# Kernel tuning notes

Hardware: AMD Instinct MI355X
Metric: run time of the kernel (lower is better)

The kernel has to match this reference:

```python
import jax, jax.numpy as jnp
import numpy as np

B, T, DIM, H = 2, 2048, 512, 8
EPS = 1e-6


def setup_inputs() -> dict:
    key = jax.random.key(0)
    ks = jax.random.split(key, 6)
    scale = 0.05  # keep activations in a sane range for softmax/elu
    return {
        "x": jax.random.normal(ks[0], (B, T, DIM), dtype=jnp.float32),
        "Wq": jax.random.normal(ks[1], (DIM, DIM), dtype=jnp.float32) * scale,
        "Wk": jax.random.normal(ks[2], (DIM, DIM), dtype=jnp.float32) * scale,
        "Wv": jax.random.normal(ks[3], (DIM, DIM), dtype=jnp.float32) * scale,
        "Wo": jax.random.normal(ks[4], (DIM, DIM), dtype=jnp.float32) * scale,
        "bo": jax.random.normal(ks[5], (DIM,), dtype=jnp.float32) * scale,
    }


def reference(x, Wq, Wk, Wv, Wo, bo):
    b, t, dim = x.shape
    h = H
    d = dim // h
    # projections (nn.Linear: x @ W.T)
    q = x @ Wq.T
    k = x @ Wk.T
    v = x @ Wv.T
    mh = lambda z: z.reshape(b, t, h, d).transpose(0, 2, 1, 3)  # [b,h,t,d]
    q, k, v = mh(q), mh(k), mh(v)
    # causal linear attention with buckets = n (bucket size 1, no shift)
    q = jax.nn.softmax(q, axis=-1)
    k = jax.nn.elu(k) + 1.0  # psi
    k_cumsum = jnp.cumsum(k, axis=2)                       # [b,h,t,d]
    context = jnp.einsum('bhnd,bhne->bhnde', k, v)         # per-position outer products
    context = jnp.cumsum(context, axis=2)                  # causal prefix sum, [b,h,t,d,d]
    context = context / (k_cumsum[..., None] + EPS)        # safe_div
    attn = jnp.einsum('bhnd,bhnde->bhne', q, context)      # [b,h,t,d]
    out = attn.transpose(0, 2, 1, 3).reshape(b, t, dim)
    return out @ Wo.T + bo
```

## Files before the change

### kernel.cpp

```cpp
#include <hip/hip_runtime.h>

#define T_SEQ 2048
#define DIMM 512
#define NH 8
#define HD 64
#define BB 2
#define CHUNK 64
#define NCHUNK 32
#define EPSV 1e-6f
#define LDST 72
#define CST 132

typedef __attribute__((ext_vector_type(8))) short bf16x8;
typedef __attribute__((ext_vector_type(4))) short s16x4;
typedef __attribute__((ext_vector_type(4))) float f32x4;

static __device__ inline short f2bf(float f) {
    union { float f; unsigned u; } v; v.f = f;
    unsigned r = v.u + 0x7FFFu + ((v.u >> 16) & 1u);
    return (short)(r >> 16);
}
static __device__ inline float bf2f(short s) {
    union { unsigned u; float f; } v; v.u = ((unsigned)(unsigned short)s) << 16;
    return v.f;
}
static __device__ __forceinline__ void gload_lds16(const void* g, void* l) {
    __builtin_amdgcn_global_load_lds(
        (__attribute__((address_space(1))) void*)g,
        (__attribute__((address_space(3))) void*)l, 16, 0, 0);
}

__global__ __launch_bounds__(256) void convert_kernel(
    const float* __restrict__ x, const float* __restrict__ Wq,
    const float* __restrict__ Wk, const float* __restrict__ Wv,
    const float* __restrict__ Wo,
    short* __restrict__ xb, short* __restrict__ Wcat, short* __restrict__ Wob)
{
    const int u = blockIdx.x * 256 + threadIdx.x;
    const float* src; short* dst;
    if (u < 262144) {
        src = x + (size_t)u * 8; dst = xb + (size_t)u * 8;
    } else {
        const int v = u - 262144;
        const int o = (v & 32767) * 8;
        if (v < 32768)       { src = Wq + o; dst = Wcat + o; }
        else if (v < 65536)  { src = Wk + o; dst = Wcat + 262144 + o; }
        else if (v < 98304)  { src = Wv + o; dst = Wcat + 524288 + o; }
        else                 { src = Wo + o; dst = Wob + o; }
    }
    const float4 a = *(const float4*)src;
    const float4 b = *(const float4*)(src + 4);
    *(bf16x8*)dst = (bf16x8){f2bf(a.x), f2bf(a.y), f2bf(a.z), f2bf(a.w),
                             f2bf(b.x), f2bf(b.y), f2bf(b.z), f2bf(b.w)};
}

__global__ __launch_bounds__(256) void proj_mfma_kernel(
    const short* __restrict__ xb, const short* __restrict__ Wcat,
    short* __restrict__ Qs, short* __restrict__ Kbf,
    short* __restrict__ Ktb, short* __restrict__ Vt)
{
    __shared__ short S[64 * 64 + 128 * 64];
    short* As = S;
    short* Bs = S + 4096;
    short* Cs = S;
    const int m0 = blockIdx.x * 64;
    const int n0 = blockIdx.y * 128;
    const int which = blockIdx.y >> 2;
    const int tid = threadIdx.x;
    const int lane = tid & 63, w = tid >> 6;
    const int wr = w >> 1, wc = w & 1;
    const int fr = lane & 15, fg = lane >> 4;
    const int lr = lane >> 3, lc = (lane & 7) * 8;
    f32x4 acc[2][4] = {};
    for (int k0 = 0; k0 < DIMM; k0 += 64) {
        #pragma unroll
        for (int it = 0; it < 2; it++) {
            const int r0 = w * 16 + it * 8;
            gload_lds16(xb + (size_t)(m0 + r0 + lr) * DIMM + k0 + lc, &As[r0 * 64]);
        }
        #pragma unroll
        for (int it = 0; it < 4; it++) {
            const int r0 = w * 32 + it * 8;
            gload_lds16(Wcat + (size_t)(n0 + r0 + lr) * DIMM + k0 + lc, &Bs[r0 * 64]);
        }
        __syncthreads();
        #pragma unroll
        for (int ks = 0; ks < 2; ks++) {
            bf16x8 af[2], bfr[4];
            #pragma unroll
            for (int i = 0; i < 2; i++)
                af[i] = *(const bf16x8*)&As[(wr * 32 + i * 16 + fr) * 64 + ks * 32 + fg * 8];
            #pragma unroll
            for (int j = 0; j < 4; j++)
                bfr[j] = *(const bf16x8*)&Bs[(wc * 64 + j * 16 + fr) * 64 + ks * 32 + fg * 8];
            #pragma unroll
            for (int i = 0; i < 2; i++)
                #pragma unroll
                for (int j = 0; j < 4; j++)
                    acc[i][j] = __builtin_amdgcn_mfma_f32_16x16x32_bf16(af[i], bfr[j], acc[i][j], 0, 0, 0);
        }
        __syncthreads();
    }
    #pragma unroll
    for (int i = 0; i < 2; i++)
        #pragma unroll
        for (int j = 0; j < 4; j++)
            #pragma unroll
            for (int reg = 0; reg < 4; reg++) {
                float val = acc[i][j][reg];
                if (which == 1) val = (val > 0.f) ? (val + 1.f) : __expf(val);
                Cs[(wr * 32 + i * 16 + fg * 4 + reg) * CST + wc * 64 + j * 16 + fr] = f2bf(val);
            }
    __syncthreads();

    const int b = m0 >> 11, t0 = m0 & (T_SEQ - 1);
    if (which == 0) {
        if (tid < 128) {
            const int r = tid & 63, hh = tid >> 6;
            const int head = (blockIdx.y & 3) * 2 + hh;
            s16x4 seg[16];
            #pragma unroll
            for (int s = 0; s < 16; s++) seg[s] = *(const s16x4*)&Cs[r * CST + hh * 64 + s * 4];
            float mx = -1e30f;
            #pragma unroll
            for (int s = 0; s < 16; s++)
                #pragma unroll
                for (int k = 0; k < 4; k++) mx = fmaxf(mx, bf2f(seg[s][k]));
            float sum = 0.f;
            #pragma unroll
            for (int s = 0; s < 16; s++)
                #pragma unroll
                for (int k = 0; k < 4; k++) sum += __expf(bf2f(seg[s][k]) - mx);
            const float inv = 1.f / sum;
            short* qp = Qs + (((size_t)(b * NH + head)) * T_SEQ + t0 + r) * HD;
            #pragma unroll
            for (int s = 0; s < 16; s += 2) {
                bf16x8 o;
                #pragma unroll
                for (int k = 0; k < 4; k++) o[k] = f2bf(__expf(bf2f(seg[s][k]) - mx) * inv);
                #pragma unroll
                for (int k = 0; k < 4; k++) o[4 + k] = f2bf(__expf(bf2f(seg[s + 1][k]) - mx) * inv);
                *(bf16x8*)(qp + s * 4) = o;
            }
        }
    } else if (which == 1) {
        if (tid < 128) {
            const int r = tid & 63, hh = tid >> 6;
            const int head = (blockIdx.y & 3) * 2 + hh;
            short* kp = Kbf + (((size_t)(b * NH + head)) * T_SEQ + t0 + r) * HD;
            #pragma unroll
            for (int s = 0; s < 8; s++) {
                const s16x4 a = *(const s16x4*)&Cs[r * CST + hh * 64 + s * 8];
                const s16x4 bq = *(const s16x4*)&Cs[r * CST + hh * 64 + s * 8 + 4];
                *(bf16x8*)(kp + s * 8) = (bf16x8){a[0], a[1], a[2], a[3], bq[0], bq[1], bq[2], bq[3]};
            }
        }
        {
            const int c = tid & 127, half = tid >> 7;
            const int head = (blockIdx.y & 3) * 2 + (c >> 6);
            const int d = c & 63;
            short* ktp = Ktb + (((size_t)(b * NH + head)) * HD + d) * T_SEQ + t0 + half * 32;
            #pragma unroll
            for (int s = 0; s < 4; s++) {
                bf16x8 o;
                #pragma unroll
                for (int k = 0; k < 8; k++) o[k] = Cs[(half * 32 + s * 8 + k) * CST + c];
                *(bf16x8*)(ktp + s * 8) = o;
            }
        }
    } else {
        const int c = tid & 127, half = tid >> 7;
        const int head = (blockIdx.y & 3) * 2 + (c >> 6);
        const int e = c & 63;
        short* vtp = Vt + (((size_t)(b * NH + head)) * HD + e) * T_SEQ + t0 + half * 32;
        #pragma unroll
        for (int s = 0; s < 4; s++) {
            bf16x8 o;
            #pragma unroll
            for (int k = 0; k < 8; k++) o[k] = Cs[(half * 32 + s * 8 + k) * CST + c];
            *(bf16x8*)(vtp + s * 8) = o;
        }
    }
}

__global__ __launch_bounds__(256) void chunk_sum_kernel(
    const short* __restrict__ Ktb, const short* __restrict__ Vt,
    float* __restrict__ Schunk, float* __restrict__ kchunk)
{
    __shared__ short VtL[64 * LDST];
    __shared__ short KtL[64 * LDST];
    __shared__ float ksp[4][64];
    const int bh = blockIdx.x >> 5, c = blockIdx.x & 31;
    const int tid = threadIdx.x;
    const int lane = tid & 63, w = tid >> 6;
    const int fr = lane & 15, fg = lane >> 4;
    #pragma unroll
    for (int it = 0; it < 2; it++) {
        const int qi = it * 256 + tid;
        const int r = qi >> 3, c8 = (qi & 7) * 8;
        *(bf16x8*)&VtL[r * LDST + c8] =
            *(const bf16x8*)(Vt + ((size_t)(bh * HD) + r) * T_SEQ + c * CHUNK + c8);
        *(bf16x8*)&KtL[r * LDST + c8] =
            *(const bf16x8*)(Ktb + ((size_t)(bh * HD) + r) * T_SEQ + c * CHUNK + c8);
    }
    __syncthreads();
    f32x4 acc[4] = {};
    #pragma unroll
    for (int ks = 0; ks < 2; ks++) {
        const bf16x8 av = *(const bf16x8*)&VtL[(w * 16 + fr) * LDST + ks * 32 + fg * 8];
        #pragma unroll
        for (int j = 0; j < 4; j++) {
            const bf16x8 bk = *(const bf16x8*)&KtL[(j * 16 + fr) * LDST + ks * 32 + fg * 8];
            acc[j] = __builtin_amdgcn_mfma_f32_16x16x32_bf16(av, bk, acc[j], 0, 0, 0);
        }
    }
    float* Sout = Schunk + ((size_t)bh * NCHUNK + c) * 4096;
    #pragma unroll
    for (int j = 0; j < 4; j++)
        #pragma unroll
        for (int reg = 0; reg < 4; reg++)
            Sout[(w * 16 + fg * 4 + reg) * 64 + j * 16 + fr] = acc[j][reg];
    float ps = 0.f;
    #pragma unroll
    for (int t = 0; t < 16; t++) ps += bf2f(KtL[lane * LDST + w * 16 + t]);
    ksp[w][lane] = ps;
    __syncthreads();
    if (tid < 64)
        kchunk[((size_t)bh * NCHUNK + c) * 64 + tid] =
            ksp[0][tid] + ksp[1][tid] + ksp[2][tid] + ksp[3][tid];
}

__global__ __launch_bounds__(256) void scan_kernel(float* __restrict__ Schunk,
                                                   float* __restrict__ kchunk)
{
    const int gid = blockIdx.x * 256 + threadIdx.x;
    if (blockIdx.x < 256) {
        const int bh = gid >> 12, i = gid & 4095;
        float run = 0.f;
        float* p = Schunk + (size_t)bh * NCHUNK * 4096 + i;
        for (int c = 0; c < NCHUNK; c++) { const float tv = p[c * 4096]; p[c * 4096] = run; run += tv; }
    } else {
        const int idx = gid - 65536;
        const int bh = idx >> 6, d = idx & 63;
        float run = 0.f;
        float* p = kchunk + (size_t)bh * NCHUNK * 64 + d;
        for (int c = 0; c < NCHUNK; c++) { const float tv = p[c * 64]; p[c * 64] = run; run += tv; }
    }
}

__global__ __launch_bounds__(256) void intra_kernel(
    const short* __restrict__ Qs, const short* __restrict__ Kbf,
    const short* __restrict__ Vt, const float* __restrict__ Schunk,
    const float* __restrict__ kchunk, short* __restrict__ attnb)
{
    __shared__ short B1[64 * LDST];
    __shared__ short B2[64 * LDST];
    __shared__ short KL[64 * LDST];
    __shared__ short VtL[64 * LDST];
    __shared__ short QnL[64 * LDST];
    __shared__ float gsum[4][64];
    __shared__ float kpre[64];
    const int bh = blockIdx.x >> 5, c = blockIdx.x & 31;
    const int tid = threadIdx.x;
    const int lane = tid & 63, w = tid >> 6;
    const int fr = lane & 15, fg = lane >> 4;
    const size_t tdbase = ((size_t)bh * T_SEQ + c * CHUNK) * HD;
    #pragma unroll
    for (int it = 0; it < 2; it++) {
        const int qi = it * 256 + tid;
        const int r = qi >> 3, c8 = (qi & 7) * 8;
        *(bf16x8*)&B1[r * LDST + c8]  = *(const bf16x8*)(Qs + tdbase + r * HD + c8);
        *(bf16x8*)&KL[r * LDST + c8]  = *(const bf16x8*)(Kbf + tdbase + r * HD + c8);
        *(bf16x8*)&VtL[r * LDST + c8] =
            *(const bf16x8*)(Vt + ((size_t)(bh * HD) + r) * T_SEQ + c * CHUNK + c8);
    }
    {
        const float* Sp = Schunk + ((size_t)bh * NCHUNK + c) * 4096;
        #pragma unroll
        for (int it = 0; it < 4; it++) {
            const int qi = it * 256 + tid;
            const int r = qi >> 4, c4 = (qi & 15) * 4;
            const float4 v = *(const float4*)(Sp + r * 64 + c4);
            *(s16x4*)&B2[r * LDST + c4] = (s16x4){f2bf(v.x), f2bf(v.y), f2bf(v.z), f2bf(v.w)};
        }
    }
    if (tid < 64) kpre[tid] = kchunk[((size_t)bh * NCHUNK + c) * 64 + tid];
    __syncthreads();
    {
        float s = 0.f;
        #pragma unroll
        for (int t = 0; t < 16; t++) s += bf2f(KL[(w * 16 + t) * LDST + lane]);
        gsum[w][lane] = s;
    }
    __syncthreads();
    {
        float run = kpre[lane];
        for (int gg = 0; gg < w; gg++) run += gsum[gg][lane];
        #pragma unroll
        for (int t0 = 0; t0 < 16; t0++) {
            const int t = w * 16 + t0;
            run += bf2f(KL[t * LDST + lane]);
            const float qv = bf2f(B1[t * LDST + lane]);
            QnL[t * LDST + lane] = f2bf(qv / (run + EPSV));
        }
    }
    __syncthreads();
    {
        f32x4 a1[4] = {};
        #pragma unroll
        for (int ks = 0; ks < 2; ks++) {
            const bf16x8 aq = *(const bf16x8*)&QnL[(w * 16 + fr) * LDST + ks * 32 + fg * 8];
            #pragma unroll
            for (int j = 0; j < 4; j++) {
                const bf16x8 bk = *(const bf16x8*)&KL[(j * 16 + fr) * LDST + ks * 32 + fg * 8];
                a1[j] = __builtin_amdgcn_mfma_f32_16x16x32_bf16(aq, bk, a1[j], 0, 0, 0);
            }
        }
        const int trow = w * 16 + fg * 4;
        #pragma unroll
        for (int j = 0; j < 4; j++)
            #pragma unroll
            for (int reg = 0; reg < 4; reg++) {
                const int t = trow + reg, s = j * 16 + fr;
                B1[t * LDST + s] = (s <= t) ? f2bf(a1[j][reg]) : (short)0;
            }
    }
    __syncthreads();
    {
        f32x4 a2[4] = {};
        #pragma unroll
        for (int ks = 0; ks < 2; ks++) {
            const bf16x8 aq = *(const bf16x8*)&QnL[(w * 16 + fr) * LDST + ks * 32 + fg * 8];
            const bf16x8 aa = *(const bf16x8*)&B1[(w * 16 + fr) * LDST + ks * 32 + fg * 8];
            #pragma unroll
            for (int j = 0; j < 4; j++) {
                const bf16x8 bs = *(const bf16x8*)&B2[(j * 16 + fr) * LDST + ks * 32 + fg * 8];
                const bf16x8 bv = *(const bf16x8*)&VtL[(j * 16 + fr) * LDST + ks * 32 + fg * 8];
                a2[j] = __builtin_amdgcn_mfma_f32_16x16x32_bf16(aq, bs, a2[j], 0, 0, 0);
                a2[j] = __builtin_amdgcn_mfma_f32_16x16x32_bf16(aa, bv, a2[j], 0, 0, 0);
            }
        }
        short* ap = attnb + tdbase;
        const int trow = w * 16 + fg * 4;
        #pragma unroll
        for (int j = 0; j < 4; j++)
            #pragma unroll
            for (int reg = 0; reg < 4; reg++)
                ap[(trow + reg) * HD + j * 16 + fr] = f2bf(a2[j][reg]);
    }
}

__global__ __launch_bounds__(256) void outproj_mfma_kernel(
    const short* __restrict__ attnb, const short* __restrict__ Wob,
    const float* __restrict__ bo, float* __restrict__ out)
{
    __shared__ short As[64 * 64];
    __shared__ short Bs[64 * 64];
    const int m0 = blockIdx.x * 64;
    const int n0 = blockIdx.y * 64;
    const int tid = threadIdx.x;
    const int lane = tid & 63, w = tid >> 6;
    const int fr = lane & 15, fg = lane >> 4;
    const int lr = lane >> 3, lc = (lane & 7) * 8;
    const int b = m0 >> 11, tbase = m0 & (T_SEQ - 1);
    f32x4 acc[4] = {};
    for (int k0 = 0; k0 < DIMM; k0 += 64) {
        const int h = k0 >> 6;
        #pragma unroll
        for (int it = 0; it < 2; it++) {
            const int r0 = w * 16 + it * 8;
            gload_lds16(attnb + (((size_t)(b * NH + h)) * T_SEQ + tbase + r0 + lr) * HD + lc,
                        &As[r0 * 64]);
            gload_lds16(Wob + (size_t)(n0 + r0 + lr) * DIMM + k0 + lc, &Bs[r0 * 64]);
        }
        __syncthreads();
        #pragma unroll
        for (int ks = 0; ks < 2; ks++) {
            const bf16x8 af = *(const bf16x8*)&As[(w * 16 + fr) * 64 + ks * 32 + fg * 8];
            #pragma unroll
            for (int j = 0; j < 4; j++) {
                const bf16x8 bfr = *(const bf16x8*)&Bs[(j * 16 + fr) * 64 + ks * 32 + fg * 8];
                acc[j] = __builtin_amdgcn_mfma_f32_16x16x32_bf16(af, bfr, acc[j], 0, 0, 0);
            }
        }
        __syncthreads();
    }
    #pragma unroll
    for (int j = 0; j < 4; j++)
        #pragma unroll
        for (int reg = 0; reg < 4; reg++) {
            const int m = m0 + w * 16 + fg * 4 + reg;
            const int n = n0 + j * 16 + fr;
            out[(size_t)m * DIMM + n] = acc[j][reg] + bo[n];
        }
}

extern "C" void kernel_launch(void* const* d_in, const int* in_sizes, int n_in,
                              void* d_out, int out_size, void* d_ws, size_t ws_size,
                              hipStream_t stream)
{
    const float* x  = (const float*)d_in[0];
    const float* Wq = (const float*)d_in[1];
    const float* Wk = (const float*)d_in[2];
    const float* Wv = (const float*)d_in[3];
    const float* Wo = (const float*)d_in[4];
    const float* bo = (const float*)d_in[5];
    float* out = (float*)d_out;

    const size_t NELEM = (size_t)BB * T_SEQ * DIMM;
    short* xb    = (short*)d_ws;
    short* Wcat  = xb + NELEM;
    short* Wob   = Wcat + 786432;
    short* Qs    = Wob + 262144;
    short* Kbf   = Qs + NELEM;
    short* Ktb   = Kbf + NELEM;
    short* Vt    = Ktb + NELEM;
    short* attnb = Vt + NELEM;
    float* Schunk = (float*)(attnb + NELEM);
    float* kchunk = Schunk + (size_t)BB * NH * NCHUNK * 4096;

    convert_kernel<<<dim3(1536), 256, 0, stream>>>(x, Wq, Wk, Wv, Wo, xb, Wcat, Wob);
    proj_mfma_kernel<<<dim3(64, 12), 256, 0, stream>>>(xb, Wcat, Qs, Kbf, Ktb, Vt);
    chunk_sum_kernel<<<dim3(BB * NH * NCHUNK), 256, 0, stream>>>(Ktb, Vt, Schunk, kchunk);
    scan_kernel<<<dim3(260), 256, 0, stream>>>(Schunk, kchunk);
    intra_kernel<<<dim3(BB * NH * NCHUNK), 256, 0, stream>>>(Qs, Kbf, Vt, Schunk, kchunk, attnb);
    outproj_mfma_kernel<<<dim3(64, 8), 256, 0, stream>>>(attnb, Wob, bo, out);
}
```

Before: 58.63 us.

## Double-buffer projection GEMM LDS tiles and XOR-swizzle columns to avoid bank conflicts

The projection GEMM now keeps two LDS buffers. It issues global-to-LDS loads for the next K tile while MFMAs run on the current one, so each step needs one barrier instead of two. The LDS column index is also XOR-swizzled by row, which is meant to remove bank conflicts on the fragment reads. LDS use per block grows to about 48KB, which may lower occupancy. The loads also rely on the async global_load_lds finishing before the single barrier.

```diff
diff --git a/kernel.cpp b/kernel.cpp
--- a/kernel.cpp
+++ b/kernel.cpp
@@ -10,6 +10,7 @@
 #define EPSV 1e-6f
 #define LDST 72
 #define CST 132
+#define PBUF 12288
 
 typedef __attribute__((ext_vector_type(8))) short bf16x8;
 typedef __attribute__((ext_vector_type(4))) short s16x4;
@@ -59,9 +60,7 @@
     short* __restrict__ Qs, short* __restrict__ Kbf,
     short* __restrict__ Ktb, short* __restrict__ Vt)
 {
-    __shared__ short S[64 * 64 + 128 * 64];
-    short* As = S;
-    short* Bs = S + 4096;
+    __shared__ short S[2 * PBUF];
     short* Cs = S;
     const int m0 = blockIdx.x * 64;
     const int n0 = blockIdx.y * 128;
@@ -70,29 +69,54 @@
     const int lane = tid & 63, w = tid >> 6;
     const int wr = w >> 1, wc = w & 1;
     const int fr = lane & 15, fg = lane >> 4;
-    const int lr = lane >> 3, lc = (lane & 7) * 8;
+    const int lrr = lane >> 3;
+    const int sl8 = ((lane & 7) ^ lrr) * 8;
+    const int xr = fr & 7;
     f32x4 acc[2][4] = {};
-    for (int k0 = 0; k0 < DIMM; k0 += 64) {
+
+    {
+        short* As = S; short* Bs = S + 4096;
         #pragma unroll
         for (int it = 0; it < 2; it++) {
             const int r0 = w * 16 + it * 8;
-            gload_lds16(xb + (size_t)(m0 + r0 + lr) * DIMM + k0 + lc, &As[r0 * 64]);
+            gload_lds16(xb + (size_t)(m0 + r0 + lrr) * DIMM + sl8, &As[r0 * 64]);
         }
         #pragma unroll
         for (int it = 0; it < 4; it++) {
             const int r0 = w * 32 + it * 8;
-            gload_lds16(Wcat + (size_t)(n0 + r0 + lr) * DIMM + k0 + lc, &Bs[r0 * 64]);
-        }
-        __syncthreads();
+            gload_lds16(Wcat + (size_t)(n0 + r0 + lrr) * DIMM + sl8, &Bs[r0 * 64]);
+        }
+    }
+    __syncthreads();
+
+    for (int t = 0; t < 8; t++) {
+        const int cur = t & 1;
+        if (t < 7) {
+            const int k0 = (t + 1) * 64;
+            short* As = S + (cur ^ 1) * PBUF;
+            short* Bs = As + 4096;
+            #pragma unroll
+            for (int it = 0; it < 2; it++) {
+                const int r0 = w * 16 + it * 8;
+                gload_lds16(xb + (size_t)(m0 + r0 + lrr) * DIMM + k0 + sl8, &As[r0 * 64]);
+            }
+            #pragma unroll
+            for (int it = 0; it < 4; it++) {
+                const int r0 = w * 32 + it * 8;
+                gload_lds16(Wcat + (size_t)(n0 + r0 + lrr) * DIMM + k0 + sl8, &Bs[r0 * 64]);
+            }
+        }
+        const short* As = S + cur * PBUF;
+        const short* Bs = As + 4096;
         #pragma unroll
         for (int ks = 0; ks < 2; ks++) {
             bf16x8 af[2], bfr[4];
             #pragma unroll
             for (int i = 0; i < 2; i++)
-                af[i] = *(const bf16x8*)&As[(wr * 32 + i * 16 + fr) * 64 + ks * 32 + fg * 8];
+                af[i] = *(const bf16x8*)&As[(wr * 32 + i * 16 + fr) * 64 + (((ks << 2) + fg) ^ xr) * 8];
             #pragma unroll
             for (int j = 0; j < 4; j++)
-                bfr[j] = *(const bf16x8*)&Bs[(wc * 64 + j * 16 + fr) * 64 + ks * 32 + fg * 8];
+                bfr[j] = *(const bf16x8*)&Bs[(wc * 64 + j * 16 + fr) * 64 + (((ks << 2) + fg) ^ xr) * 8];
             #pragma unroll
             for (int i = 0; i < 2; i++)
                 #pragma unroll
@@ -101,6 +125,7 @@
         }
         __syncthreads();
     }
+
     #pragma unroll
     for (int i = 0; i < 2; i++)
         #pragma unroll
```

Result: faster. 54.97 us (-6.2%).

## Double-buffer projection GEMM LDS loads and XOR-swizzle tiles to avoid bank conflicts

Applied to the files above, without the earlier changes.

Rewrites the K loop of the QKV projection MFMA kernel to double-buffer A/B tiles in LDS. The next two stages are prefetched with direct global-to-LDS loads, and explicit vmcnt waits let memory traffic overlap the MFMA work. It also XOR-swizzles the 16-byte column chunks on store and read to reduce LDS bank conflicts. LDS use rises to two 12288-short buffers, which may lower occupancy, and the hand-written waitcnt counts depend on the exact number of loads issued per stage.

```diff
diff --git a/kernel.cpp b/kernel.cpp
--- a/kernel.cpp
+++ b/kernel.cpp
@@ -10,6 +10,7 @@
 #define EPSV 1e-6f
 #define LDST 72
 #define CST 132
+#define PBUF 12288
 
 typedef __attribute__((ext_vector_type(8))) short bf16x8;
 typedef __attribute__((ext_vector_type(4))) short s16x4;
@@ -59,9 +60,7 @@
     short* __restrict__ Qs, short* __restrict__ Kbf,
     short* __restrict__ Ktb, short* __restrict__ Vt)
 {
-    __shared__ short S[64 * 64 + 128 * 64];
-    short* As = S;
-    short* Bs = S + 4096;
+    __shared__ short S[2 * PBUF];
     short* Cs = S;
     const int m0 = blockIdx.x * 64;
     const int n0 = blockIdx.y * 128;
@@ -70,37 +69,66 @@
     const int lane = tid & 63, w = tid >> 6;
     const int wr = w >> 1, wc = w & 1;
     const int fr = lane & 15, fg = lane >> 4;
-    const int lr = lane >> 3, lc = (lane & 7) * 8;
+    const int lrr = lane >> 3;
+    const int sl8 = ((lane & 7) ^ lrr) * 8;
+    const int xr = fr & 7;
     f32x4 acc[2][4] = {};
-    for (int k0 = 0; k0 < DIMM; k0 += 64) {
-        #pragma unroll
-        for (int it = 0; it < 2; it++) {
-            const int r0 = w * 16 + it * 8;
-            gload_lds16(xb + (size_t)(m0 + r0 + lr) * DIMM + k0 + lc, &As[r0 * 64]);
-        }
-        #pragma unroll
-        for (int it = 0; it < 4; it++) {
-            const int r0 = w * 32 + it * 8;
-            gload_lds16(Wcat + (size_t)(n0 + r0 + lr) * DIMM + k0 + lc, &Bs[r0 * 64]);
-        }
-        __syncthreads();
-        #pragma unroll
-        for (int ks = 0; ks < 2; ks++) {
-            bf16x8 af[2], bfr[4];
-            #pragma unroll
-            for (int i = 0; i < 2; i++)
-                af[i] = *(const bf16x8*)&As[(wr * 32 + i * 16 + fr) * 64 + ks * 32 + fg * 8];
-            #pragma unroll
-            for (int j = 0; j < 4; j++)
-                bfr[j] = *(const bf16x8*)&Bs[(wc * 64 + j * 16 + fr) * 64 + ks * 32 + fg * 8];
-            #pragma unroll
-            for (int i = 0; i < 2; i++)
+
+    #define STAGE(buf, k0)                                                       \
+        {                                                                        \
+            short* As_ = S + (buf) * PBUF;                                       \
+            short* Bs_ = As_ + 4096;                                             \
+            _Pragma("unroll")                                                    \
+            for (int it = 0; it < 2; it++) {                                     \
+                const int r0 = w * 16 + it * 8;                                  \
+                gload_lds16(xb + (size_t)(m0 + r0 + lrr) * DIMM + (k0) + sl8,    \
+                            &As_[r0 * 64]);                                      \
+            }                                                                    \
+            _Pragma("unroll")                                                    \
+            for (int it = 0; it < 4; it++) {                                     \
+                const int r0 = w * 32 + it * 8;                                  \
+                gload_lds16(Wcat + (size_t)(n0 + r0 + lrr) * DIMM + (k0) + sl8,  \
+                            &Bs_[r0 * 64]);                                      \
+            }                                                                    \
+        }
+
+    STAGE(0, 0);
+    STAGE(1, 64);
+
+    #pragma unroll
+    for (int t = 0; t < 8; t++) {
+        if (t < 7) asm volatile("s_waitcnt vmcnt(6)" ::: "memory");
+        else       asm volatile("s_waitcnt vmcnt(0)" ::: "memory");
+        __builtin_amdgcn_sched_barrier(0);
+        __builtin_amdgcn_s_barrier();
+        __builtin_amdgcn_sched_barrier(0);
+        {
+            const short* As = S + (t & 1) * PBUF;
+            const short* Bs = As + 4096;
+            #pragma unroll
+            for (int ks = 0; ks < 2; ks++) {
+                const int cc = (((ks << 2) + fg) ^ xr) * 8;
+                bf16x8 af[2], bfr[4];
+                #pragma unroll
+                for (int i = 0; i < 2; i++)
+                    af[i] = *(const bf16x8*)&As[(wr * 32 + i * 16 + fr) * 64 + cc];
                 #pragma unroll
                 for (int j = 0; j < 4; j++)
-                    acc[i][j] = __builtin_amdgcn_mfma_f32_16x16x32_bf16(af[i], bfr[j], acc[i][j], 0, 0, 0);
-        }
-        __syncthreads();
-    }
+                    bfr[j] = *(const bf16x8*)&Bs[(wc * 64 + j * 16 + fr) * 64 + cc];
+                #pragma unroll
+                for (int i = 0; i < 2; i++)
+                    #pragma unroll
+                    for (int j = 0; j < 4; j++)
+                        acc[i][j] = __builtin_amdgcn_mfma_f32_16x16x32_bf16(af[i], bfr[j], acc[i][j], 0, 0, 0);
+            }
+        }
+        __builtin_amdgcn_sched_barrier(0);
+        __builtin_amdgcn_s_barrier();
+        __builtin_amdgcn_sched_barrier(0);
+        if (t < 6) STAGE(t & 1, (t + 2) * 64);
+    }
+    #undef STAGE
+
     #pragma unroll
     for (int i = 0; i < 2; i++)
         #pragma unroll
```

Measured after the change: 54.82 us, median of 2. -6.5%, faster.
